# Kernel tuning notes

Measured on AMD Instinct MI355X. Metric: run time of the kernel, lower is better.

Reference implementation:

```python
import jax, jax.numpy as jnp
import numpy as np

LN_EPS = 1e-5
SN_EPS = 1e-12


def _block(x, W, b, g, be):
    # Linear -> LayerNorm -> CELU, fused as one expression chain
    h = x @ W.T + b
    mu = jnp.mean(h, axis=-1, keepdims=True)
    var = jnp.mean(jnp.square(h - mu), axis=-1, keepdims=True)
    h = (h - mu) * jax.lax.rsqrt(var + LN_EPS) * g + be
    return jax.nn.celu(h)


def _spectral_norm_weight(W, u):
    # One power iteration (torch training-mode behavior), u/v detached.
    v = W.T @ u
    v = v / (jnp.linalg.norm(v) + SN_EPS)
    u2 = W @ v
    u2 = u2 / (jnp.linalg.norm(u2) + SN_EPS)
    sigma = u2 @ (W @ v)
    return W / sigma


def setup_inputs() -> dict:
    key = jax.random.key(0)
    ks = jax.random.split(key, 8)
    B, D = 131072, 512
    sizes = [512, 128, 32, 8]
    inp = {"x": jax.random.normal(ks[0], (B, D), dtype=jnp.float32)}
    fan_in = D
    for i, s in enumerate(sizes, start=1):
        scale = 1.0 / np.sqrt(fan_in)
        inp[f"W{i}"] = jax.random.normal(ks[i], (s, fan_in), dtype=jnp.float32) * scale
        inp[f"b{i}"] = jnp.zeros((s,), dtype=jnp.float32)
        inp[f"g{i}"] = jnp.ones((s,), dtype=jnp.float32)
        inp[f"be{i}"] = jnp.zeros((s,), dtype=jnp.float32)
        fan_in = s
    inp["Wh"] = jax.random.normal(ks[5], (1, 8), dtype=jnp.float32) * (1.0 / np.sqrt(8))
    inp["bh"] = jnp.zeros((1,), dtype=jnp.float32)
    inp["u"] = jax.random.normal(ks[6], (1,), dtype=jnp.float32)
    return inp


def reference(x, W1, b1, g1, be1, W2, b2, g2, be2, W3, b3, g3, be3,
              W4, b4, g4, be4, Wh, bh, u):
    h = _block(x, W1, b1, g1, be1)
    h = _block(h, W2, b2, g2, be2)
    h = _block(h, W3, b3, g3, be3)
    h = _block(h, W4, b4, g4, be4)          # hidden_output: [B, 8]
    Wsn = _spectral_norm_weight(Wh, u)
    return h @ Wsn.T + bh                   # [B, 1]
```

## Files before the change

kernel.cpp:

```cpp
#include <hip/hip_runtime.h>


typedef unsigned short u16;
typedef unsigned int   u32;
typedef __bf16  bf16x8 __attribute__((ext_vector_type(8)));
typedef float   f32x16 __attribute__((ext_vector_type(16)));

__device__ __forceinline__ u16 f2bf(float f) {
    u32 x = __builtin_bit_cast(u32, f);
    x += 0x7FFFu + ((x >> 16) & 1u);
    return (u16)(x >> 16);
}
__device__ __forceinline__ float bfval(u16 h) { return __builtin_bit_cast(float, (u32)h << 16); }
__device__ __forceinline__ u32 pack2(float a, float b) { return (u32)f2bf(a) | ((u32)f2bf(b) << 16); }
__device__ __forceinline__ float celu1(float x) { return x > 0.f ? x : __expf(x) - 1.f; }

#define W1F_OFF 0
#define W2F_OFF 262144
#define W3F_OFF 327680
#define W3LF_OFF 331776
#define NGROUPS 41984

__global__ void prep_weights(const float* __restrict__ W1, const float* __restrict__ W2,
                             const float* __restrict__ W3, u16* __restrict__ wsb) {
    const int g = blockIdx.x * 256 + threadIdx.x;
    if (g < 32768) {
        const int l = g & 63, t = (g >> 6) & 15, ksg = g >> 10;
        const int n = t * 32 + (l & 31);
        const int k0 = ksg * 16 + (l >> 5) * 8;
        u16* dst = wsb + W1F_OFF + g * 8;
        const float* src = W1 + n * 512 + k0;
#pragma unroll
        for (int e = 0; e < 8; ++e) dst[e] = f2bf(src[e]);
    } else if (g < 40960) {
        const int h = g - 32768;
        const int l = h & 63, t = (h >> 6) & 3, ksg = h >> 8;
        const int n = t * 32 + (l & 31);
        const int k0 = ksg * 16 + (l >> 5) * 8;
        u16* dst = wsb + W2F_OFF + h * 8;
        const float* src = W2 + n * 512 + k0;
#pragma unroll
        for (int e = 0; e < 8; ++e) dst[e] = f2bf(src[e]);
    } else if (g < 41472) {
        const int h = g - 40960;
        const int l = h & 63, ksg = h >> 6;
        const int n = l & 31;
        const int k0 = ksg * 16 + (l >> 5) * 8;
        u16* dst = wsb + W3F_OFF + h * 8;
        const float* src = W3 + n * 128 + k0;
#pragma unroll
        for (int e = 0; e < 8; ++e) dst[e] = f2bf(src[e]);
    } else {
        const int h = g - 41472;
        const int l = h & 63, ksg = h >> 6;
        const int n = l & 31;
        const int k0 = ksg * 16 + (l >> 5) * 8;
        u16* dst = wsb + W3LF_OFF + h * 8;
        const float* src = W3 + n * 128 + k0;
#pragma unroll
        for (int e = 0; e < 8; ++e) { float w = src[e]; dst[e] = f2bf(w - bfval(f2bf(w))); }
    }
}

#define PW4 0
#define PB4 256
#define PG4 264
#define PBE4 272
#define PWH 280
#define PBH 288
#define PU  289
#define NPAR 290

__global__ __launch_bounds__(512, 4) void fused_mlp(
    const float* __restrict__ x,
    const u16* __restrict__ W1b, const u16* __restrict__ W2b,
    const u16* __restrict__ W3b, const u16* __restrict__ W3Lb,
    const float* __restrict__ b1, const float* __restrict__ g1, const float* __restrict__ be1,
    const float* __restrict__ b2, const float* __restrict__ g2, const float* __restrict__ be2,
    const float* __restrict__ b3, const float* __restrict__ g3, const float* __restrict__ be3,
    const float* __restrict__ W4, const float* __restrict__ b4, const float* __restrict__ g4,
    const float* __restrict__ be4,
    const float* __restrict__ Wh, const float* __restrict__ bh, const float* __restrict__ uvec,
    float* __restrict__ out)
{
    __shared__ __align__(16) u16 sXH[64][520];
    __shared__ __align__(16) float sPS[64][8];
    __shared__ __align__(16) float sPQ[64][8];
    __shared__ __align__(8)  float2 sMR[64];
    __shared__ __align__(16) float sP[NPAR + 2];

    const int tid = threadIdx.x;
    const int wv = tid >> 6;
    const int lane = tid & 63;
    const int ln = lane & 31;
    const int lh = lane >> 5;
    const int Ng = wv;
    const int row0 = blockIdx.x * 64;

    const float b1a = b1[Ng * 64 + ln],  b1c = b1[Ng * 64 + 32 + ln];
    const float g1a = g1[Ng * 64 + ln],  g1c = g1[Ng * 64 + 32 + ln];
    const float e1a = be1[Ng * 64 + ln], e1c = be1[Ng * 64 + 32 + ln];
    const int Mt2 = wv >> 2, Nt2 = wv & 3;
    const float b2v = b2[Nt2 * 32 + ln], g2v = g2[Nt2 * 32 + ln], e2v = be2[Nt2 * 32 + ln];
    const float b3v = b3[ln], g3v = g3[ln], e3v = be3[ln];

    if (tid < NPAR) {
        float v;
        if      (tid < 256) v = W4[tid];
        else if (tid < 264) v = b4[tid - 256];
        else if (tid < 272) v = g4[tid - 264];
        else if (tid < 280) v = be4[tid - 272];
        else if (tid < 288) v = Wh[tid - 280];
        else if (tid == 288) v = bh[0];
        else                v = uvec[0];
        sP[tid] = v;
    }

    {
        const float4* xp = (const float4*)(x) + (long)blockIdx.x * 8192 + tid;
        float4 q[16];
#pragma unroll
        for (int j = 0; j < 16; ++j) q[j] = xp[j * 512];
        const int r0 = tid >> 7;
        const int c4 = (tid & 127) * 4;
#pragma unroll
        for (int j = 0; j < 16; ++j)
            *(uint2*)(&sXH[j * 4 + r0][c4]) =
                make_uint2(pack2(q[j].x, q[j].y), pack2(q[j].z, q[j].w));
    }
    __syncthreads();

    f32x16 acc[2][2] = {};
    {
        const u16* wq = W1b + (Ng * 2) * 512 + lane * 8;
        bf16x8 Bf[4][2];
#pragma unroll
        for (int s = 0; s < 3; ++s) {
            Bf[s][0] = *(const bf16x8*)(wq + s * 8192);
            Bf[s][1] = *(const bf16x8*)(wq + s * 8192 + 512);
        }
#pragma unroll
        for (int ksg = 0; ksg < 32; ++ksg) {
            const int slot = ksg & 3;
            if (ksg + 3 < 32) {
                const int ps = (ksg + 3) & 3;
                const u16* np = wq + (ksg + 3) * 8192;
                Bf[ps][0] = *(const bf16x8*)(np);
                Bf[ps][1] = *(const bf16x8*)(np + 512);
            }
            bf16x8 a0 = *(const bf16x8*)(&sXH[ln][ksg * 16 + lh * 8]);
            bf16x8 a1 = *(const bf16x8*)(&sXH[32 + ln][ksg * 16 + lh * 8]);
            acc[0][0] = __builtin_amdgcn_mfma_f32_32x32x16_bf16(a0, Bf[slot][0], acc[0][0], 0, 0, 0);
            acc[0][1] = __builtin_amdgcn_mfma_f32_32x32x16_bf16(a0, Bf[slot][1], acc[0][1], 0, 0, 0);
            acc[1][0] = __builtin_amdgcn_mfma_f32_32x32x16_bf16(a1, Bf[slot][0], acc[1][0], 0, 0, 0);
            acc[1][1] = __builtin_amdgcn_mfma_f32_32x32x16_bf16(a1, Bf[slot][1], acc[1][1], 0, 0, 0);
        }
    }

#pragma unroll
    for (int rg = 0; rg < 16; ++rg) {
        acc[0][0][rg] += b1a; acc[0][1][rg] += b1c;
        acc[1][0][rg] += b1a; acc[1][1][rg] += b1c;
    }
#pragma unroll
    for (int mt = 0; mt < 2; ++mt)
#pragma unroll
    for (int rg = 0; rg < 16; ++rg) {
        float s = acc[mt][0][rg] + acc[mt][1][rg];
        float q = acc[mt][0][rg] * acc[mt][0][rg] + acc[mt][1][rg] * acc[mt][1][rg];
#pragma unroll
        for (int m = 1; m < 32; m <<= 1) { s += __shfl_xor(s, m, 64); q += __shfl_xor(q, m, 64); }
        if (ln == 0) {
            const int row = mt * 32 + (rg & 3) + 8 * (rg >> 2) + 4 * lh;
            sPS[row][Ng] = s; sPQ[row][Ng] = q;
        }
    }
    __syncthreads();
    if (tid < 64) {
        float s = 0.f, q = 0.f;
#pragma unroll
        for (int j = 0; j < 8; ++j) { s += sPS[tid][j]; q += sPQ[tid][j]; }
        const float mu = s * (1.f / 512.f);
        const float var = q * (1.f / 512.f) - mu * mu;
        sMR[tid] = make_float2(mu, rsqrtf(var + 1e-5f));
    }
    __syncthreads();
#pragma unroll
    for (int mt = 0; mt < 2; ++mt)
#pragma unroll
    for (int rg = 0; rg < 16; ++rg) {
        const int row = mt * 32 + (rg & 3) + 8 * (rg >> 2) + 4 * lh;
        const float2 mr = sMR[row];
        const float h0 = (acc[mt][0][rg] - mr.x) * mr.y * g1a + e1a;
        const float h1v = (acc[mt][1][rg] - mr.x) * mr.y * g1c + e1c;
        sXH[row][Ng * 64 + ln] = f2bf(celu1(h0));
        sXH[row][Ng * 64 + 32 + ln] = f2bf(celu1(h1v));
    }
    __syncthreads();

    float v2[16];
    {
        const u16* w2q = W2b + Nt2 * 512 + lane * 8;
        bf16x8 W2f[4];
#pragma unroll
        for (int s = 0; s < 4; ++s) W2f[s] = *(const bf16x8*)(w2q + s * 2048);
        f32x16 a2 = {}, a2b = {};
        const u16* h1p = &sXH[Mt2 * 32 + ln][lh * 8];
#pragma unroll
        for (int ksg = 0; ksg < 32; ++ksg) {
            const int slot = ksg & 3;
            bf16x8 af = *(const bf16x8*)(h1p + ksg * 16);
            if (ksg & 1) a2b = __builtin_amdgcn_mfma_f32_32x32x16_bf16(af, W2f[slot], a2b, 0, 0, 0);
            else         a2  = __builtin_amdgcn_mfma_f32_32x32x16_bf16(af, W2f[slot], a2, 0, 0, 0);
            if (ksg + 4 < 32) W2f[slot] = *(const bf16x8*)(w2q + (ksg + 4) * 2048);
        }
#pragma unroll
        for (int rg = 0; rg < 16; ++rg) v2[rg] = a2[rg] + a2b[rg] + b2v;
#pragma unroll
        for (int rg = 0; rg < 16; ++rg) {
            float s = v2[rg], q = v2[rg] * v2[rg];
#pragma unroll
            for (int m = 1; m < 32; m <<= 1) { s += __shfl_xor(s, m, 64); q += __shfl_xor(q, m, 64); }
            if (ln == 0) {
                const int row = Mt2 * 32 + (rg & 3) + 8 * (rg >> 2) + 4 * lh;
                sPS[row][Nt2] = s; sPQ[row][Nt2] = q;
            }
        }
    }
    __syncthreads();
    if (tid < 64) {
        float s = sPS[tid][0] + sPS[tid][1] + sPS[tid][2] + sPS[tid][3];
        float q = sPQ[tid][0] + sPQ[tid][1] + sPQ[tid][2] + sPQ[tid][3];
        const float mu = s * (1.f / 128.f);
        const float var = q * (1.f / 128.f) - mu * mu;
        sMR[tid] = make_float2(mu, rsqrtf(var + 1e-5f));
    }
    __syncthreads();
    {
        const int col = Nt2 * 32 + ln;
#pragma unroll
        for (int rg = 0; rg < 16; ++rg) {
            const int row = Mt2 * 32 + (rg & 3) + 8 * (rg >> 2) + 4 * lh;
            const float2 mr = sMR[row];
            const float hn = (v2[rg] - mr.x) * mr.y * g2v + e2v;
            const float a = celu1(hn);
            const u16 hi = f2bf(a);
            sXH[row][col] = hi;
            sXH[row][128 + col] = f2bf(a - bfval(hi));
        }
    }
    __syncthreads();

    if (wv < 2) {
        f32x16 a3 = {};
        const u16* w3q  = W3b  + lane * 8;
        const u16* w3lq = W3Lb + lane * 8;
        const u16* h2p  = &sXH[wv * 32 + ln][lh * 8];
        const u16* h2lp = &sXH[wv * 32 + ln][128 + lh * 8];
#pragma unroll
        for (int ks = 0; ks < 8; ++ks) {
            bf16x8 fa_h = *(const bf16x8*)(h2p  + ks * 16);
            bf16x8 fa_l = *(const bf16x8*)(h2lp + ks * 16);
            bf16x8 fb_h = *(const bf16x8*)(w3q  + ks * 512);
            bf16x8 fb_l = *(const bf16x8*)(w3lq + ks * 512);
            a3 = __builtin_amdgcn_mfma_f32_32x32x16_bf16(fa_h, fb_h, a3, 0, 0, 0);
            a3 = __builtin_amdgcn_mfma_f32_32x32x16_bf16(fa_h, fb_l, a3, 0, 0, 0);
            a3 = __builtin_amdgcn_mfma_f32_32x32x16_bf16(fa_l, fb_h, a3, 0, 0, 0);
        }
#pragma unroll
        for (int rg = 0; rg < 16; ++rg) {
            const float v = a3[rg] + b3v;
            float s = v, q = v * v;
#pragma unroll
            for (int m = 1; m < 32; m <<= 1) { s += __shfl_xor(s, m, 64); q += __shfl_xor(q, m, 64); }
            const float mu = s * (1.f / 32.f);
            const float rs = rsqrtf(q * (1.f / 32.f) - mu * mu + 1e-5f);
            const int row = wv * 32 + (rg & 3) + 8 * (rg >> 2) + 4 * lh;
            float* s3 = (float*)&sXH[row][256 * 2];
            s3 = (float*)&sXH[row][0] + 128;
            s3[ln] = celu1((v - mu) * rs * g3v + e3v);
        }
    }
    __syncthreads();

    if (tid < 256) {
        const int r = tid & 63, og = tid >> 6;
        float h[32];
        const float4* hp = (const float4*)((float*)&sXH[r][0] + 128);
#pragma unroll
        for (int j = 0; j < 8; ++j) {
            float4 tv = hp[j];
            h[j * 4 + 0] = tv.x; h[j * 4 + 1] = tv.y; h[j * 4 + 2] = tv.z; h[j * 4 + 3] = tv.w;
        }
#pragma unroll
        for (int oo = 0; oo < 2; ++oo) {
            const int o = og * 2 + oo;
            float a = sP[PB4 + o];
            const float* w4 = &sP[PW4 + o * 32];
#pragma unroll
            for (int k = 0; k < 32; ++k) a += h[k] * w4[k];
            sPS[r][o] = a;
        }
    }
    __syncthreads();

    if (tid < 64) {
        float v[8];
        float s = 0.f, q = 0.f;
#pragma unroll
        for (int o = 0; o < 8; ++o) { v[o] = sPS[tid][o]; s += v[o]; q += v[o] * v[o]; }
        const float mu = s * 0.125f;
        const float var = q * 0.125f - mu * mu;
        const float rs = rsqrtf(var + 1e-5f);

        float wh[8];
        const float u0 = sP[PU];
        float nv = 0.f;
#pragma unroll
        for (int o = 0; o < 8; ++o) { wh[o] = sP[PWH + o]; float tt = wh[o] * u0; nv += tt * tt; }
        nv = sqrtf(nv);
        const float inv = 1.f / (nv + 1e-12f);
        float s2 = 0.f;
#pragma unroll
        for (int o = 0; o < 8; ++o) s2 += wh[o] * (wh[o] * u0 * inv);
        const float u2 = s2 / (fabsf(s2) + 1e-12f);
        const float sigma = u2 * s2;
        const float isg = 1.f / sigma;

        float y = sP[PBH];
#pragma unroll
        for (int o = 0; o < 8; ++o) {
            const float hn = (v[o] - mu) * rs * sP[PG4 + o] + sP[PBE4 + o];
            y += celu1(hn) * wh[o] * isg;
        }
        out[row0 + tid] = y;
    }
}

extern "C" void kernel_launch(void* const* d_in, const int* in_sizes, int n_in,
                              void* d_out, int out_size, void* d_ws, size_t ws_size,
                              hipStream_t stream) {
    const float* x   = (const float*)d_in[0];
    const float* W1  = (const float*)d_in[1];
    const float* b1  = (const float*)d_in[2];
    const float* g1  = (const float*)d_in[3];
    const float* be1 = (const float*)d_in[4];
    const float* W2  = (const float*)d_in[5];
    const float* b2  = (const float*)d_in[6];
    const float* g2  = (const float*)d_in[7];
    const float* be2 = (const float*)d_in[8];
    const float* W3  = (const float*)d_in[9];
    const float* b3  = (const float*)d_in[10];
    const float* g3  = (const float*)d_in[11];
    const float* be3 = (const float*)d_in[12];
    const float* W4  = (const float*)d_in[13];
    const float* b4  = (const float*)d_in[14];
    const float* g4  = (const float*)d_in[15];
    const float* be4 = (const float*)d_in[16];
    const float* Wh  = (const float*)d_in[17];
    const float* bh  = (const float*)d_in[18];
    const float* u   = (const float*)d_in[19];
    float* out = (float*)d_out;
    u16* wsb = (u16*)d_ws;

    prep_weights<<<dim3(NGROUPS / 256), dim3(256), 0, stream>>>(W1, W2, W3, wsb);

    const int rows = in_sizes[0] / 512;
    fused_mlp<<<dim3(rows / 64), dim3(512), 0, stream>>>(
        x, wsb + W1F_OFF, wsb + W2F_OFF, wsb + W3F_OFF, wsb + W3LF_OFF,
        b1, g1, be1, b2, g2, be2, b3, g3, be3,
        W4, b4, g4, be4, Wh, bh, u, out);
}
```

Before: 547.0 us.

## Fuse layer-4 tail into per-wave path, add MFMA priority, use native bf16 convert

The tail of the kernel is restructured so that each of the two remaining waves computes layer 4, its LayerNorm and the head for its own 32 rows. This removes two block-wide barriers and the shared-memory round trip through sPS, and lets the other waves exit early. The MFMA loops for layers 1 and 2 are wrapped in s_setprio to raise wave priority, and the manual round-to-nearest bf16 conversion is replaced with the compiler's native cast. Having one wave do all 8 outputs serialises more FMA work per lane. It also depends on a wave-local s_waitcnt being enough to order its own LDS writes before the reads.

Result: no change. 539.3 us (-1.4%).

```diff
diff --git a/kernel.cpp b/kernel.cpp
--- a/kernel.cpp
+++ b/kernel.cpp
@@ -7,9 +7,7 @@
 typedef float   f32x16 __attribute__((ext_vector_type(16)));
 
 __device__ __forceinline__ u16 f2bf(float f) {
-    u32 x = __builtin_bit_cast(u32, f);
-    x += 0x7FFFu + ((x >> 16) & 1u);
-    return (u16)(x >> 16);
+    return __builtin_bit_cast(u16, (__bf16)f);
 }
 __device__ __forceinline__ float bfval(u16 h) { return __builtin_bit_cast(float, (u32)h << 16); }
 __device__ __forceinline__ u32 pack2(float a, float b) { return (u32)f2bf(a) | ((u32)f2bf(b) << 16); }
@@ -139,6 +137,7 @@
             Bf[s][0] = *(const bf16x8*)(wq + s * 8192);
             Bf[s][1] = *(const bf16x8*)(wq + s * 8192 + 512);
         }
+        __builtin_amdgcn_s_setprio(1);
 #pragma unroll
         for (int ksg = 0; ksg < 32; ++ksg) {
             const int slot = ksg & 3;
@@ -155,6 +154,7 @@
             acc[1][0] = __builtin_amdgcn_mfma_f32_32x32x16_bf16(a1, Bf[slot][0], acc[1][0], 0, 0, 0);
             acc[1][1] = __builtin_amdgcn_mfma_f32_32x32x16_bf16(a1, Bf[slot][1], acc[1][1], 0, 0, 0);
         }
+        __builtin_amdgcn_s_setprio(0);
     }
 
 #pragma unroll
@@ -206,6 +206,7 @@
         for (int s = 0; s < 4; ++s) W2f[s] = *(const bf16x8*)(w2q + s * 2048);
         f32x16 a2 = {}, a2b = {};
         const u16* h1p = &sXH[Mt2 * 32 + ln][lh * 8];
+        __builtin_amdgcn_s_setprio(1);
 #pragma unroll
         for (int ksg = 0; ksg < 32; ++ksg) {
             const int slot = ksg & 3;
@@ -214,6 +215,7 @@
             else         a2  = __builtin_amdgcn_mfma_f32_32x32x16_bf16(af, W2f[slot], a2, 0, 0, 0);
             if (ksg + 4 < 32) W2f[slot] = *(const bf16x8*)(w2q + (ksg + 4) * 2048);
         }
+        __builtin_amdgcn_s_setprio(0);
 #pragma unroll
         for (int rg = 0; rg < 16; ++rg) v2[rg] = a2[rg] + a2b[rg] + b2v;
 #pragma unroll
@@ -251,7 +253,9 @@
     }
     __syncthreads();
 
-    if (wv < 2) {
+    if (wv >= 2) return;
+
+    {
         f32x16 a3 = {};
         const u16* w3q  = W3b  + lane * 8;
         const u16* w3lq = W3Lb + lane * 8;
@@ -276,39 +280,31 @@
             const float mu = s * (1.f / 32.f);
             const float rs = rsqrtf(q * (1.f / 32.f) - mu * mu + 1e-5f);
             const int row = wv * 32 + (rg & 3) + 8 * (rg >> 2) + 4 * lh;
-            float* s3 = (float*)&sXH[row][256 * 2];
-            s3 = (float*)&sXH[row][0] + 128;
+            float* s3 = (float*)&sXH[row][0] + 128;
             s3[ln] = celu1((v - mu) * rs * g3v + e3v);
         }
     }
-    __syncthreads();
-
-    if (tid < 256) {
-        const int r = tid & 63, og = tid >> 6;
+    __asm__ volatile("s_waitcnt lgkmcnt(0)" ::: "memory");
+
+    if (lane < 32) {
+        const int r = wv * 32 + lane;
         float h[32];
-        const float4* hp = (const float4*)((float*)&sXH[r][0] + 128);
+        const float4* hp = (const float4*)((const float*)&sXH[r][0] + 128);
 #pragma unroll
         for (int j = 0; j < 8; ++j) {
             float4 tv = hp[j];
             h[j * 4 + 0] = tv.x; h[j * 4 + 1] = tv.y; h[j * 4 + 2] = tv.z; h[j * 4 + 3] = tv.w;
         }
-#pragma unroll
-        for (int oo = 0; oo < 2; ++oo) {
-            const int o = og * 2 + oo;
+        float v[8];
+        float s = 0.f, q = 0.f;
+#pragma unroll
+        for (int o = 0; o < 8; ++o) {
             float a = sP[PB4 + o];
             const float* w4 = &sP[PW4 + o * 32];
 #pragma unroll
             for (int k = 0; k < 32; ++k) a += h[k] * w4[k];
-            sPS[r][o] = a;
-        }
-    }
-    __syncthreads();
-
-    if (tid < 64) {
-        float v[8];
-        float s = 0.f, q = 0.f;
-#pragma unroll
-        for (int o = 0; o < 8; ++o) { v[o] = sPS[tid][o]; s += v[o]; q += v[o] * v[o]; }
+            v[o] = a; s += a; q += a * a;
+        }
         const float mu = s * 0.125f;
         const float var = q * 0.125f - mu * mu;
         const float rs = rsqrtf(var + 1e-5f);
@@ -333,7 +329,7 @@
             const float hn = (v[o] - mu) * rs * sP[PG4 + o] + sP[PBE4 + o];
             y += celu1(hn) * wh[o] * isg;
         }
-        out[row0 + tid] = y;
+        out[row0 + r] = y;
     }
 }
 
```
